# Optimization experiments

Hardware: AMD Instinct MI355X
Metric: run time of the kernel (lower is better)

Reference implementation:

```python
import jax, jax.numpy as jnp
import numpy as np

B, T, ENC, TAG, HG, HE, M = 64, 383, 768, 128, 400, 256, 20
D = ENC + TAG          # graph RNN input size (encoder_output_dim + tag_representation_dim)
S = T + 1              # +1 for head sentinel


def setup_inputs() -> dict:
    ks = jax.random.split(jax.random.key(0), 16)
    g = lambda i, shape, s=0.05: jax.random.normal(ks[i], shape, dtype=jnp.float32) * s
    z = lambda n: jnp.zeros((n,), jnp.float32)
    return dict(
        input=g(0, (B, T, ENC), 1.0),
        tag_embeddings=g(1, (B, T, TAG), 1.0),
        mask=jnp.ones((B, T), jnp.int32),
        head_sentinel=g(2, (D,), 1.0),
        # bidirectional graph RNN (tanh, 1 layer)
        Wih_f=g(3, (HG, D)), Whh_f=g(4, (HG, HG)), bih_f=z(HG), bhh_f=z(HG),
        Wih_b=g(5, (HG, D)), Whh_b=g(6, (HG, HG)), bih_b=z(HG), bhh_b=z(HG),
        # graph_to_edge projection (edge RNN initial hidden)
        Wg2e=g(7, (HE, 2 * HG)), bg2e=z(HE),
        # edge RNN (past direction, input size 1) + edge classifier head
        Wih_e=g(8, (HE, 1)), Whh_e=g(9, (HE, HE)), bih_e=z(HE), bhh_e=z(HE),
        Wcls=g(10, (1, HE)), bcls=z(1),
        bos=z(1),
        # head/dep tag feedforwards
        Wht=g(11, (TAG, 2 * HG)), bht=z(TAG),
        Wdt=g(12, (TAG, 2 * HG)), bdt=z(TAG),
    )


def _masked_rnn(x, m, Wih, Whh, bih, bhh, reverse):
    # x: [B,S,D], m: [B,S,1]. Emulates packed nn.RNN(tanh) for one direction:
    # hidden only advances on valid steps (so the backward direction starts its
    # recurrence at each sequence's true length), outputs are zero on padding
    # (matching pad_packed_sequence zero padding).
    def step(h, inp):
        xt, mt = inp
        hn = jnp.tanh(xt @ Wih.T + bih + h @ Whh.T + bhh)
        h = mt * hn + (1.0 - mt) * h
        return h, h * mt

    h0 = jnp.zeros((x.shape[0], Wih.shape[0]), x.dtype)
    _, ys = jax.lax.scan(step, h0, (x.swapaxes(0, 1), m.swapaxes(0, 1)), reverse=reverse)
    return ys.swapaxes(0, 1)


def reference(input, tag_embeddings, mask, head_sentinel,
              Wih_f, Whh_f, bih_f, bhh_f, Wih_b, Whh_b, bih_b, bhh_b,
              Wg2e, bg2e, Wih_e, Whh_e, bih_e, bhh_e, Wcls, bcls, bos,
              Wht, bht, Wdt, bdt):
    x = jnp.concatenate([input, tag_embeddings], axis=-1)            # [B,T,D]
    sent = jnp.broadcast_to(head_sentinel, (B, 1, D))
    x = jnp.concatenate([sent, x], axis=1)                           # [B,S,D]
    m = jnp.concatenate([jnp.ones((B, 1), mask.dtype), mask], axis=1)  # sentinel is valid
    mf = m.astype(x.dtype)[..., None]                                # [B,S,1]

    fwd = _masked_rnn(x, mf, Wih_f, Whh_f, bih_f, bhh_f, reverse=False)
    bwd = _masked_rnn(x, mf, Wih_b, Whh_b, bih_b, bhh_b, reverse=True)
    graph_state = jnp.concatenate([fwd, bwd], axis=-1)               # [B,S,2*HG]

    # initial hidden = graph_to_edge(graph_state), input starts at bos, then
    # feeds back the previous logit.
    proj = graph_state.reshape(B * S, 2 * HG) @ Wg2e.T + bg2e        # [B*S,HE]
    steps = min(M, S)
    x0 = jnp.broadcast_to(bos.reshape(1, 1), (B * S, 1))

    def estep(carry, _):
        xe, h = carry
        hn = jnp.tanh(xe @ Wih_e.T + bih_e + h @ Whh_e.T + bhh_e)
        logit = hn @ Wcls.T + bcls                                   # [B*S,1]
        return (logit, hn), logit

    _, logits = jax.lax.scan(estep, (x0, proj), None, length=steps)  # [steps,B*S,1]
    Ap = logits.squeeze(-1).T.reshape(B, S, steps)                   # [B,S,steps]

    # banded scatter: arc_logits[:, i, start:i] = Ap[:, i, :i-start], start=max(0,i-M)
    rows = jnp.arange(S)[:, None]
    cols = jnp.arange(S)[None, :]
    start = jnp.maximum(0, rows - M)
    k = cols - start
    valid = (cols >= start) & (cols < rows)
    idx = jnp.clip(k, 0, steps - 1)
    band = Ap[:, jnp.broadcast_to(rows, (S, S)), jnp.broadcast_to(idx, (S, S))]  # [B,S,S]
    arc_logits = jnp.where(valid[None], band, jnp.zeros((), Ap.dtype))

    # tag feedforwards (Dropout is identity in eval)
    head_tag = jax.nn.elu(graph_state @ Wht.T + bht)
    dep_tag = jax.nn.elu(graph_state @ Wdt.T + bdt)
    return head_tag, dep_tag, arc_logits
```

## Files before the change

kernel.cpp:

```cpp
#include <hip/hip_runtime.h>

#define B_ 64
#define T_ 383
#define S_ 384
#define ENC_ 768
#define TAGD_ 128
#define D_ 896
#define HG_ 400
#define HE_ 256
#define MSTEP_ 20
#define RTOT_ (B_*S_)
#define HEAD_SZ_ ((size_t)RTOT_*TAGD_)

typedef short short8 __attribute__((ext_vector_type(8)));
typedef float f32x4 __attribute__((ext_vector_type(4)));

__device__ __forceinline__ float bf2f(unsigned short u){
  union { unsigned int i; float f; } v; v.i = ((unsigned int)u) << 16; return v.f;
}
__device__ __forceinline__ unsigned short f2bf(float f){
  union { float f; unsigned int i; } v; v.f = f;
  unsigned int r = (v.i + 0x7fffu + ((v.i >> 16) & 1u)) >> 16;
  return (unsigned short)r;
}
__device__ __forceinline__ float tanh_fast(float x){
  float xc = fminf(fmaxf(x, -15.f), 15.f);
  float e = __expf(2.f*xc);
  return (e - 1.f) * __builtin_amdgcn_rcpf(e + 1.f);
}

__device__ __forceinline__ void probe_maps(int lane, int* mlab, int* nlab){
  unsigned short lb = f2bf((float)(lane & 15));
  short8 av, bv;
  #pragma unroll
  for (int j = 0; j < 8; j++){ av[j] = (short)lb; bv[j] = (short)0x3F80; }
  f32x4 z = {0.f,0.f,0.f,0.f};
  f32x4 d1 = __builtin_amdgcn_mfma_f32_16x16x32_bf16(av, bv, z, 0, 0, 0);
  f32x4 d2 = __builtin_amdgcn_mfma_f32_16x16x32_bf16(bv, av, z, 0, 0, 0);
  #pragma unroll
  for (int i = 0; i < 4; i++){
    mlab[i] = (int)(d1[i]*0.03125f + 0.5f);
    nlab[i] = (int)(d2[i]*0.03125f + 0.5f);
  }
}

__global__ __launch_bounds__(256) void cvt4(const float* __restrict__ src,
                                            unsigned short* __restrict__ dst, int n4)
{
  int i = blockIdx.x*256 + threadIdx.x;
  if (i >= n4) return;
  float4 v = ((const float4*)src)[i];
  ((ushort4*)dst)[i] = make_ushort4(f2bf(v.x), f2bf(v.y), f2bf(v.z), f2bf(v.w));
}

__global__ __launch_bounds__(256) void pack_wrnn3(const float* __restrict__ Wf,
                                                  const float* __restrict__ Wb,
                                                  unsigned short* __restrict__ Wr)
{
  int idx = blockIdx.x*256 + threadIdx.x;
  if (idx >= 2*26*13*16*32) return;
  int dir = idx / (26*13*16*32);
  int rem = idx % (26*13*16*32);
  int tile = rem / (13*16*32); rem %= (13*16*32);
  int kt = rem / (16*32);      rem %= (16*32);
  int r  = rem / 32;
  int kk = rem % 32;
  int n = tile*16 + r, k = kt*32 + kk;
  unsigned short v = 0;
  if (n < HG_ && k < HG_) v = f2bf((dir ? Wb : Wf)[(size_t)n*HG_ + k]);
  Wr[idx] = v;
}

__global__ __launch_bounds__(64) void maskpack(const int* __restrict__ mask,
                                               unsigned long long* __restrict__ mb)
{
  int t = blockIdx.x; int b = threadIdx.x;
  int m = (t > 0) ? mask[b*T_ + (t-1)] : 1;
  unsigned long long v = __ballot(m != 0);
  if (b == 0) mb[t] = v;
}

__global__ __launch_bounds__(256) void gemm_pre(
    const float* __restrict__ inp, const float* __restrict__ tag,
    const float* __restrict__ sent, const unsigned short* __restrict__ W,
    const float* __restrict__ bihf, const float* __restrict__ bhhf,
    const float* __restrict__ bihb, const float* __restrict__ bhhb,
    unsigned short* __restrict__ preT2)
{
  int wid = blockIdx.x*4 + (threadIdx.x >> 6);
  int lane = threadIdx.x & 63;
  int q = lane >> 4, l16 = lane & 15;
  int mt = wid / 25, ct = wid % 25;
  int r = mt*16 + l16;
  int s = r % S_, b = r / S_;
  int mlab[4], nlab[4];
  probe_maps(lane, mlab, nlab);
  int n0 = ct*32 + l16, n1 = n0 + 16;
  const unsigned short* w0 = W + (size_t)n0*D_;
  const unsigned short* w1 = W + (size_t)n1*D_;
  f32x4 acc0 = {0.f,0.f,0.f,0.f}, acc1 = {0.f,0.f,0.f,0.f};
  for (int k0 = 0; k0 < D_; k0 += 32){
    int k = k0 + q*8;
    const float* asrc = (s == 0) ? (sent + k)
        : ((k < ENC_) ? inp + (size_t)(b*T_ + (s-1))*ENC_ + k
                      : tag + (size_t)(b*T_ + (s-1))*TAGD_ + (k - ENC_));
    float4 v0 = *(const float4*)asrc;
    float4 v1 = *(const float4*)(asrc + 4);
    short8 a;
    a[0]=(short)f2bf(v0.x); a[1]=(short)f2bf(v0.y); a[2]=(short)f2bf(v0.z); a[3]=(short)f2bf(v0.w);
    a[4]=(short)f2bf(v1.x); a[5]=(short)f2bf(v1.y); a[6]=(short)f2bf(v1.z); a[7]=(short)f2bf(v1.w);
    acc0 = __builtin_amdgcn_mfma_f32_16x16x32_bf16(a, *(const short8*)(w0 + k), acc0, 0,0,0);
    acc1 = __builtin_amdgcn_mfma_f32_16x16x32_bf16(a, *(const short8*)(w1 + k), acc1, 0,0,0);
  }
  #pragma unroll
  for (int i = 0; i < 4; i++){
    int row = mt*16 + mlab[i];
    int c0 = ct*32 + nlab[i], c1 = c0 + 16;
    int bb = row / S_, ss = row % S_;
    int mtb = bb >> 4, qb = (bb >> 2) & 3, rib = bb & 3;
    float v0 = acc0[i] + ((c0 < HG_) ? (bihf[c0] + bhhf[c0]) : (bihb[c0-HG_] + bhhb[c0-HG_]));
    float v1 = acc1[i] + ((c1 < HG_) ? (bihf[c1] + bhhf[c1]) : (bihb[c1-HG_] + bhhb[c1-HG_]));
    {
      int d = (c0 >= HG_) ? 1 : 0; int nn = c0 - d*HG_;
      int nt = nn >> 4, lc = nn & 15;
      preT2[((((size_t)(d*S_ + ss)*25 + nt)*4 + mtb)*64 + (qb*16 + lc))*4 + rib] = f2bf(v0);
    }
    {
      int d = (c1 >= HG_) ? 1 : 0; int nn = c1 - d*HG_;
      int nt = nn >> 4, lc = nn & 15;
      preT2[((((size_t)(d*S_ + ss)*25 + nt)*4 + mtb)*64 + (qb*16 + lc))*4 + rib] = f2bf(v1);
    }
  }
}

#define HSTR5_ 424
template<int NTC>
__device__ void rnn_body5(int nt0, int dir, int bg, int lane, int tid,
    const unsigned short* __restrict__ pD,
    const unsigned short* __restrict__ Wd,
    const unsigned long long* __restrict__ mbits,
    unsigned short* __restrict__ gs,
    unsigned short (*Hh)[HSTR5_], unsigned short (*Hl)[HSTR5_])
{
  int q = lane >> 4, l16 = lane & 15;
  const unsigned short* wrow[NTC];
  #pragma unroll
  for (int j = 0; j < NTC; j++)
    wrow[j] = Wd + (size_t)(nt0 + j)*13*512 + l16*32 + q*8;

  short8 bh[NTC][6];
  #pragma unroll
  for (int j = 0; j < NTC; j++)
    #pragma unroll
    for (int kt = 0; kt < 6; kt++)
      bh[j][kt] = *(const short8*)(wrow[j] + kt*512);

  for (int stp = 0; stp < S_; stp++){
    int t = dir ? (S_ - 1 - stp) : stp;
    unsigned long long mb = mbits[t];
    bool allm = (mb == 0xFFFFFFFFFFFFFFFFull);
    const unsigned short* pT = pD + (size_t)t*25600;

    ushort4 pu[NTC];
    #pragma unroll
    for (int j = 0; j < NTC; j++)
      pu[j] = *(const ushort4*)(pT + (((size_t)(nt0 + j)*4 + bg)*64 + lane)*4);

    f32x4 acc[NTC];
    #pragma unroll
    for (int j = 0; j < NTC; j++) acc[j] = (f32x4){0.f,0.f,0.f,0.f};

    #pragma unroll
    for (int kt = 6; kt < 13; kt++){
      short8 bv[NTC];
      #pragma unroll
      for (int j = 0; j < NTC; j++) bv[j] = *(const short8*)(wrow[j] + kt*512);
      short8 ah = *(const short8*)&Hh[l16][kt*32 + q*8];
      short8 al = *(const short8*)&Hl[l16][kt*32 + q*8];
      #pragma unroll
      for (int j = 0; j < NTC; j++){
        acc[j] = __builtin_amdgcn_mfma_f32_16x16x32_bf16(ah, bv[j], acc[j], 0,0,0);
        acc[j] = __builtin_amdgcn_mfma_f32_16x16x32_bf16(al, bv[j], acc[j], 0,0,0);
      }
    }
    #pragma unroll
    for (int kt = 0; kt < 6; kt++){
      short8 ah = *(const short8*)&Hh[l16][kt*32 + q*8];
      short8 al = *(const short8*)&Hl[l16][kt*32 + q*8];
      #pragma unroll
      for (int j = 0; j < NTC; j++){
        acc[j] = __builtin_amdgcn_mfma_f32_16x16x32_bf16(ah, bh[j][kt], acc[j], 0,0,0);
        acc[j] = __builtin_amdgcn_mfma_f32_16x16x32_bf16(al, bh[j][kt], acc[j], 0,0,0);
      }
    }

    __syncthreads();

    #pragma unroll
    for (int j = 0; j < NTC; j++){
      int n = (nt0 + j)*16 + l16;
      unsigned short pv[4] = {pu[j].x, pu[j].y, pu[j].z, pu[j].w};
      #pragma unroll
      for (int ri = 0; ri < 4; ri++){
        int b = q*4 + ri;
        float hn = tanh_fast(acc[j][ri] + bf2f(pv[ri]));
        float hnew;
        if (allm) hnew = hn;
        else {
          bool mv = (mb >> (bg*16 + b)) & 1ull;
          float hold = bf2f(Hh[b][n]) + bf2f(Hl[b][n]);
          hnew = mv ? hn : hold;
        }
        unsigned short hi = f2bf(hnew);
        Hh[b][n] = hi;
        Hl[b][n] = f2bf(hnew - bf2f(hi));
      }
    }
    __syncthreads();

    for (int c = tid; c < 800; c += 512){
      int b = c / 50, off = c - b*50;
      uint4 dv = *(const uint4*)&Hh[b][off*8];
      bool mv = (mb >> (bg*16 + b)) & 1ull;
      uint4 z = make_uint4(0,0,0,0);
      *(uint4*)(gs + (size_t)((bg*16 + b)*S_ + t)*800 + dir*HG_ + off*8) = mv ? dv : z;
    }
  }
}

__global__ __launch_bounds__(512, 1) void rnn_mfma5(
    const unsigned short* __restrict__ preT2, const unsigned short* __restrict__ Wr,
    const unsigned long long* __restrict__ mbits, unsigned short* __restrict__ gs)
{
  __shared__ __align__(16) unsigned short Hh[16][HSTR5_];
  __shared__ __align__(16) unsigned short Hl[16][HSTR5_];
  int tid = threadIdx.x;
  int wave = tid >> 6, lane = tid & 63;
  int dir = blockIdx.x >> 2, bg = blockIdx.x & 3;
  for (int i = tid; i < 16*HSTR5_/2; i += 512){
    ((unsigned int*)Hh)[i] = 0u;
    ((unsigned int*)Hl)[i] = 0u;
  }
  __syncthreads();
  const unsigned short* Wd = Wr + (size_t)dir*26*13*512;
  const unsigned short* pD = preT2 + (size_t)dir*S_*25600;
  if (wave == 0) rnn_body5<4>(0,                dir, bg, lane, tid, pD, Wd, mbits, gs, Hh, Hl);
  else           rnn_body5<3>(4 + (wave-1)*3,   dir, bg, lane, tid, pD, Wd, mbits, gs, Hh, Hl);
}

__global__ __launch_bounds__(256) void gemm_proj(
    const unsigned short* __restrict__ gs, const unsigned short* __restrict__ Wg2e,
    const float* __restrict__ bg2e, float* __restrict__ proj)
{
  int wid = blockIdx.x*4 + (threadIdx.x >> 6);
  int lane = threadIdx.x & 63;
  int q = lane >> 4, l16 = lane & 15;
  int mt = wid >> 3, ct = wid & 7;
  int mlab[4], nlab[4];
  probe_maps(lane, mlab, nlab);
  const unsigned short* arow = gs + (size_t)(mt*16 + l16)*800;
  int n0 = ct*32 + l16, n1 = n0 + 16;
  const unsigned short* w0 = Wg2e + (size_t)n0*800;
  const unsigned short* w1 = Wg2e + (size_t)n1*800;
  f32x4 acc0 = {0.f,0.f,0.f,0.f}, acc1 = {0.f,0.f,0.f,0.f};
  for (int k0 = 0; k0 < 800; k0 += 32){
    int k = k0 + q*8;
    short8 a = *(const short8*)(arow + k);
    acc0 = __builtin_amdgcn_mfma_f32_16x16x32_bf16(a, *(const short8*)(w0 + k), acc0, 0,0,0);
    acc1 = __builtin_amdgcn_mfma_f32_16x16x32_bf16(a, *(const short8*)(w1 + k), acc1, 0,0,0);
  }
  #pragma unroll
  for (int i = 0; i < 4; i++){
    int row = mt*16 + mlab[i];
    int c0 = ct*32 + nlab[i], c1 = c0 + 16;
    proj[(size_t)row*HE_ + c0] = acc0[i] + bg2e[c0];
    proj[(size_t)row*HE_ + c1] = acc1[i] + bg2e[c1];
  }
}

__global__ __launch_bounds__(256) void gemm_tag(
    const unsigned short* __restrict__ gs, const unsigned short* __restrict__ Wtag,
    const float* __restrict__ bht, const float* __restrict__ bdt,
    float* __restrict__ outH)
{
  int wid = blockIdx.x*4 + (threadIdx.x >> 6);
  int lane = threadIdx.x & 63;
  int q = lane >> 4, l16 = lane & 15;
  int mt = wid >> 3, ct = wid & 7;
  int mlab[4], nlab[4];
  probe_maps(lane, mlab, nlab);
  const unsigned short* arow = gs + (size_t)(mt*16 + l16)*800;
  int n0 = ct*32 + l16, n1 = n0 + 16;
  const unsigned short* w0 = Wtag + (size_t)n0*800;
  const unsigned short* w1 = Wtag + (size_t)n1*800;
  f32x4 acc0 = {0.f,0.f,0.f,0.f}, acc1 = {0.f,0.f,0.f,0.f};
  for (int k0 = 0; k0 < 800; k0 += 32){
    int k = k0 + q*8;
    short8 a = *(const short8*)(arow + k);
    acc0 = __builtin_amdgcn_mfma_f32_16x16x32_bf16(a, *(const short8*)(w0 + k), acc0, 0,0,0);
    acc1 = __builtin_amdgcn_mfma_f32_16x16x32_bf16(a, *(const short8*)(w1 + k), acc1, 0,0,0);
  }
  #pragma unroll
  for (int i = 0; i < 4; i++){
    int row = mt*16 + mlab[i];
    int c0 = ct*32 + nlab[i], c1 = c0 + 16;
    float v0 = acc0[i] + ((c0 < TAGD_) ? bht[c0] : bdt[c0-TAGD_]);
    float v1 = acc1[i] + ((c1 < TAGD_) ? bht[c1] : bdt[c1-TAGD_]);
    v0 = (v0 > 0.f) ? v0 : expm1f(v0);
    v1 = (v1 > 0.f) ? v1 : expm1f(v1);
    if (c0 < TAGD_) outH[(size_t)row*TAGD_ + c0] = v0;
    else            outH[HEAD_SZ_ + (size_t)row*TAGD_ + (c0-TAGD_)] = v0;
    if (c1 < TAGD_) outH[(size_t)row*TAGD_ + c1] = v1;
    else            outH[HEAD_SZ_ + (size_t)row*TAGD_ + (c1-TAGD_)] = v1;
  }
}

#define EROWS_ 96
#define ESTR_ 264
__global__ __launch_bounds__(256, 1) void estep2(
    const float* __restrict__ proj, const unsigned short* __restrict__ WhhE,
    const float* __restrict__ bihE, const float* __restrict__ bhhE,
    const float* __restrict__ WihE, const float* __restrict__ Wcls,
    const float* __restrict__ bclsp, const float* __restrict__ bosp,
    float* __restrict__ Ap)
{
  __shared__ __align__(16) unsigned short H[2][EROWS_][ESTR_];
  __shared__ float lacc[4][EROWS_];
  __shared__ float xls[EROWS_];
  int tid = threadIdx.x;
  int wave = tid >> 6, lane = tid & 63, q = lane >> 4, l16 = lane & 15;
  size_t rowbase = (size_t)blockIdx.x * EROWS_;

  short8 bw[4][8];
  float bias_n[4], wcl_n[4], wih_n[4];
  #pragma unroll
  for (int nt = 0; nt < 4; nt++){
    int n = wave*64 + nt*16 + l16;
    #pragma unroll
    for (int kt = 0; kt < 8; kt++)
      bw[nt][kt] = *(const short8*)(WhhE + (size_t)n*HE_ + kt*32 + q*8);
    bias_n[nt] = bihE[n] + bhhE[n];
    wcl_n[nt]  = Wcls[n];
    wih_n[nt]  = WihE[n];
  }
  for (int i = tid; i < EROWS_*HE_; i += 256){
    int r = i >> 8, n = i & 255;
    H[0][r][n] = f2bf(proj[(rowbase + r)*HE_ + n]);
  }
  if (tid < EROWS_) xls[tid] = bosp[0];
  float bc = bclsp[0];
  __syncthreads();

  for (int stp = 0; stp < MSTEP_; stp++){
    int cur = stp & 1, nxt = cur ^ 1;
    float lp[6][4];
    #pragma unroll
    for (int mt = 0; mt < 6; mt++){
      short8 af[8];
      #pragma unroll
      for (int kt = 0; kt < 8; kt++)
        af[kt] = *(const short8*)&H[cur][mt*16 + l16][kt*32 + q*8];
      float xr[4];
      #pragma unroll
      for (int ri = 0; ri < 4; ri++) xr[ri] = xls[mt*16 + q*4 + ri];
      f32x4 acc[4];
      #pragma unroll
      for (int nt = 0; nt < 4; nt++) acc[nt] = (f32x4){0.f,0.f,0.f,0.f};
      #pragma unroll
      for (int kt = 0; kt < 8; kt++){
        #pragma unroll
        for (int nt = 0; nt < 4; nt++)
          acc[nt] = __builtin_amdgcn_mfma_f32_16x16x32_bf16(af[kt], bw[nt][kt], acc[nt], 0,0,0);
      }
      #pragma unroll
      for (int ri = 0; ri < 4; ri++) lp[mt][ri] = 0.f;
      #pragma unroll
      for (int nt = 0; nt < 4; nt++){
        int n = wave*64 + nt*16 + l16;
        #pragma unroll
        for (int ri = 0; ri < 4; ri++){
          float v = acc[nt][ri] + bias_n[nt] + xr[ri]*wih_n[nt];
          float h = tanh_fast(v);
          lp[mt][ri] += h * wcl_n[nt];
          H[nxt][mt*16 + q*4 + ri][n] = f2bf(h);
        }
      }
    }
    #pragma unroll
    for (int mt = 0; mt < 6; mt++){
      #pragma unroll
      for (int ri = 0; ri < 4; ri++){
        float v = lp[mt][ri];
        v += __shfl_xor(v, 1, 16);
        v += __shfl_xor(v, 2, 16);
        v += __shfl_xor(v, 4, 16);
        v += __shfl_xor(v, 8, 16);
        lp[mt][ri] = v;
      }
    }
    if (l16 == 0){
      #pragma unroll
      for (int mt = 0; mt < 6; mt++)
        #pragma unroll
        for (int ri = 0; ri < 4; ri++)
          lacc[wave][mt*16 + q*4 + ri] = lp[mt][ri];
    }
    __syncthreads();
    if (tid < EROWS_){
      float lg = lacc[0][tid] + lacc[1][tid] + lacc[2][tid] + lacc[3][tid] + bc;
      Ap[(rowbase + tid)*MSTEP_ + stp] = lg;
      xls[tid] = lg;
    }
    __syncthreads();
  }
}

__global__ __launch_bounds__(256) void band_kernel(const float* __restrict__ Ap,
                                                   float* __restrict__ arc)
{
  int idx = blockIdx.x*256 + threadIdx.x;
  int c = idx % S_;
  int rr = (idx / S_) % S_;
  int b = idx / (S_*S_);
  int start = rr - MSTEP_; if (start < 0) start = 0;
  bool valid = (c >= start) && (c < rr);
  float v = 0.f;
  if (valid) v = Ap[(size_t)(b*S_ + rr)*MSTEP_ + (c - start)];
  arc[idx] = v;
}

extern "C" void kernel_launch(void* const* d_in, const int* in_sizes, int n_in,
                              void* d_out, int out_size, void* d_ws, size_t ws_size,
                              hipStream_t stream)
{
  const float* inp  = (const float*)d_in[0];
  const float* tag  = (const float*)d_in[1];
  const int*   mask = (const int*)d_in[2];
  const float* sent = (const float*)d_in[3];
  const float* Wihf = (const float*)d_in[4];
  const float* Whhf = (const float*)d_in[5];
  const float* bihf = (const float*)d_in[6];
  const float* bhhf = (const float*)d_in[7];
  const float* Wihb = (const float*)d_in[8];
  const float* Whhb = (const float*)d_in[9];
  const float* bihb = (const float*)d_in[10];
  const float* bhhb = (const float*)d_in[11];
  const float* Wg2e = (const float*)d_in[12];
  const float* bg2e = (const float*)d_in[13];
  const float* WihE = (const float*)d_in[14];
  const float* WhhE = (const float*)d_in[15];
  const float* bihE = (const float*)d_in[16];
  const float* bhhE = (const float*)d_in[17];
  const float* Wcls = (const float*)d_in[18];
  const float* bcls = (const float*)d_in[19];
  const float* bos  = (const float*)d_in[20];
  const float* Wht  = (const float*)d_in[21];
  const float* bht  = (const float*)d_in[22];
  const float* Wdt  = (const float*)d_in[23];
  const float* bdt  = (const float*)d_in[24];
  (void)in_sizes; (void)n_in; (void)out_size; (void)ws_size;

  char* ws = (char*)d_ws;
  unsigned short* preT2  = (unsigned short*)ws;
  unsigned short* gs     = (unsigned short*)(ws + 39321600);
  unsigned short* Wrnn3  = (unsigned short*)(ws + 78643200);
  unsigned short* Wihcat = (unsigned short*)(ws + 79335424);
  unsigned short* Wg2e_b = (unsigned short*)(ws + 80769024);
  unsigned short* Wtag_b = (unsigned short*)(ws + 81178624);
  unsigned short* WhhE_b = (unsigned short*)(ws + 81588224);
  unsigned long long* maskb = (unsigned long long*)(ws + 81719296);
  float*          proj   = (float*)ws;
  float*          Ap     = (float*)(ws + 25165824);

  float* outH   = (float*)d_out;
  float* outArc = outH + 2*HEAD_SZ_;

  hipLaunchKernelGGL(cvt4, dim3(350), dim3(256), 0, stream, Wihf, Wihcat,           400*896/4);
  hipLaunchKernelGGL(cvt4, dim3(350), dim3(256), 0, stream, Wihb, Wihcat + 400*896, 400*896/4);
  hipLaunchKernelGGL(cvt4, dim3(200), dim3(256), 0, stream, Wg2e, Wg2e_b,           256*800/4);
  hipLaunchKernelGGL(cvt4, dim3(100), dim3(256), 0, stream, Wht,  Wtag_b,           128*800/4);
  hipLaunchKernelGGL(cvt4, dim3(100), dim3(256), 0, stream, Wdt,  Wtag_b + 128*800, 128*800/4);
  hipLaunchKernelGGL(cvt4, dim3(64),  dim3(256), 0, stream, WhhE, WhhE_b,           256*256/4);
  hipLaunchKernelGGL(pack_wrnn3, dim3(1352), dim3(256), 0, stream, Whhf, Whhb, Wrnn3);
  hipLaunchKernelGGL(maskpack, dim3(S_), dim3(64), 0, stream, mask, maskb);
  hipLaunchKernelGGL(gemm_pre, dim3(9600), dim3(256), 0, stream,
                     inp, tag, sent, Wihcat, bihf, bhhf, bihb, bhhb, preT2);
  hipLaunchKernelGGL(rnn_mfma5, dim3(8), dim3(512), 0, stream, preT2, Wrnn3, maskb, gs);
  hipLaunchKernelGGL(gemm_proj, dim3(3072), dim3(256), 0, stream, gs, Wg2e_b, bg2e, proj);
  hipLaunchKernelGGL(gemm_tag,  dim3(3072), dim3(256), 0, stream, gs, Wtag_b, bht, bdt, outH);
  hipLaunchKernelGGL(estep2, dim3(256), dim3(256), 0, stream,
                     proj, WhhE_b, bihE, bhhE, WihE, Wcls, bcls, bos, Ap);
  hipLaunchKernelGGL(band_kernel, dim3(36864), dim3(256), 0, stream, Ap, outArc);
}
```

Before: 2.284 ms.

## Remap pre-GEMM rows, XOR-swizzle RNN LDS, halve estep rows per block

The input-projection GEMM now indexes tiles time-major so each 16-row tile holds 16 batches at one timestep. That lets it write the RNN-friendly preT2 layout with one vectorized ushort4 store per column, and it uses packed hardware bf16 conversion. The recurrent kernel's LDS hidden-state arrays switch to a 512-wide stride with an XOR swizzle to avoid bank conflicts on the MFMA operand reads. The edge-RNN kernel handles 48 rows per block over twice as many blocks to improve occupancy and parallelism.

```diff
diff --git a/kernel.cpp b/kernel.cpp
--- a/kernel.cpp
+++ b/kernel.cpp
@@ -91,8 +91,8 @@
   int lane = threadIdx.x & 63;
   int q = lane >> 4, l16 = lane & 15;
   int mt = wid / 25, ct = wid % 25;
-  int r = mt*16 + l16;
-  int s = r % S_, b = r / S_;
+  int t = mt >> 2, mtb = mt & 3;
+  int b = mtb*16 + l16;
   int mlab[4], nlab[4];
   probe_maps(lane, mlab, nlab);
   int n0 = ct*32 + l16, n1 = n0 + 16;
@@ -101,46 +101,50 @@
   f32x4 acc0 = {0.f,0.f,0.f,0.f}, acc1 = {0.f,0.f,0.f,0.f};
   for (int k0 = 0; k0 < D_; k0 += 32){
     int k = k0 + q*8;
-    const float* asrc = (s == 0) ? (sent + k)
-        : ((k < ENC_) ? inp + (size_t)(b*T_ + (s-1))*ENC_ + k
-                      : tag + (size_t)(b*T_ + (s-1))*TAGD_ + (k - ENC_));
+    const float* asrc = (t == 0) ? (sent + k)
+        : ((k < ENC_) ? inp + (size_t)(b*T_ + (t-1))*ENC_ + k
+                      : tag + (size_t)(b*T_ + (t-1))*TAGD_ + (k - ENC_));
     float4 v0 = *(const float4*)asrc;
     float4 v1 = *(const float4*)(asrc + 4);
-    short8 a;
-    a[0]=(short)f2bf(v0.x); a[1]=(short)f2bf(v0.y); a[2]=(short)f2bf(v0.z); a[3]=(short)f2bf(v0.w);
-    a[4]=(short)f2bf(v1.x); a[5]=(short)f2bf(v1.y); a[6]=(short)f2bf(v1.z); a[7]=(short)f2bf(v1.w);
+    union { unsigned int u[4]; short8 s8; } au;
+    asm("v_cvt_pk_bf16_f32 %0, %1, %2" : "=v"(au.u[0]) : "v"(v0.x), "v"(v0.y));
+    asm("v_cvt_pk_bf16_f32 %0, %1, %2" : "=v"(au.u[1]) : "v"(v0.z), "v"(v0.w));
+    asm("v_cvt_pk_bf16_f32 %0, %1, %2" : "=v"(au.u[2]) : "v"(v1.x), "v"(v1.y));
+    asm("v_cvt_pk_bf16_f32 %0, %1, %2" : "=v"(au.u[3]) : "v"(v1.z), "v"(v1.w));
+    short8 a = au.s8;
     acc0 = __builtin_amdgcn_mfma_f32_16x16x32_bf16(a, *(const short8*)(w0 + k), acc0, 0,0,0);
     acc1 = __builtin_amdgcn_mfma_f32_16x16x32_bf16(a, *(const short8*)(w1 + k), acc1, 0,0,0);
   }
+  int q0 = mlab[0] >> 2;
+  float bb0 = (n0 < HG_) ? (bihf[n0] + bhhf[n0]) : (bihb[n0-HG_] + bhhb[n0-HG_]);
+  float bb1 = (n1 < HG_) ? (bihf[n1] + bhhf[n1]) : (bihb[n1-HG_] + bhhb[n1-HG_]);
+  unsigned short v0[4], v1[4];
   #pragma unroll
   for (int i = 0; i < 4; i++){
-    int row = mt*16 + mlab[i];
-    int c0 = ct*32 + nlab[i], c1 = c0 + 16;
-    int bb = row / S_, ss = row % S_;
-    int mtb = bb >> 4, qb = (bb >> 2) & 3, rib = bb & 3;
-    float v0 = acc0[i] + ((c0 < HG_) ? (bihf[c0] + bhhf[c0]) : (bihb[c0-HG_] + bhhb[c0-HG_]));
-    float v1 = acc1[i] + ((c1 < HG_) ? (bihf[c1] + bhhf[c1]) : (bihb[c1-HG_] + bhhb[c1-HG_]));
-    {
-      int d = (c0 >= HG_) ? 1 : 0; int nn = c0 - d*HG_;
-      int nt = nn >> 4, lc = nn & 15;
-      preT2[((((size_t)(d*S_ + ss)*25 + nt)*4 + mtb)*64 + (qb*16 + lc))*4 + rib] = f2bf(v0);
-    }
-    {
-      int d = (c1 >= HG_) ? 1 : 0; int nn = c1 - d*HG_;
-      int nt = nn >> 4, lc = nn & 15;
-      preT2[((((size_t)(d*S_ + ss)*25 + nt)*4 + mtb)*64 + (qb*16 + lc))*4 + rib] = f2bf(v1);
-    }
-  }
-}
-
-#define HSTR5_ 424
+    v0[mlab[i] & 3] = f2bf(acc0[i] + bb0);
+    v1[mlab[i] & 3] = f2bf(acc1[i] + bb1);
+  }
+  {
+    int d = (n0 >= HG_) ? 1 : 0; int nn = n0 - d*HG_; int nt = nn >> 4;
+    size_t slab = (((size_t)(d*S_ + t)*25 + nt)*4 + mtb)*256;
+    *(ushort4*)(preT2 + slab + (q0*16 + l16)*4) = make_ushort4(v0[0], v0[1], v0[2], v0[3]);
+  }
+  {
+    int d = (n1 >= HG_) ? 1 : 0; int nn = n1 - d*HG_; int nt = nn >> 4;
+    size_t slab = (((size_t)(d*S_ + t)*25 + nt)*4 + mtb)*256;
+    *(ushort4*)(preT2 + slab + (q0*16 + l16)*4) = make_ushort4(v1[0], v1[1], v1[2], v1[3]);
+  }
+}
+
+#define HSTR9_ 512
+#define HX(row, col) ((col) ^ (((row) & 15) << 3))
 template<int NTC>
-__device__ void rnn_body5(int nt0, int dir, int bg, int lane, int tid,
+__device__ void rnn_body9(int nt0, int dir, int bg, int lane, int tid,
     const unsigned short* __restrict__ pD,
     const unsigned short* __restrict__ Wd,
     const unsigned long long* __restrict__ mbits,
     unsigned short* __restrict__ gs,
-    unsigned short (*Hh)[HSTR5_], unsigned short (*Hl)[HSTR5_])
+    unsigned short (*Hh)[HSTR9_], unsigned short (*Hl)[HSTR9_])
 {
   int q = lane >> 4, l16 = lane & 15;
   const unsigned short* wrow[NTC];
@@ -175,8 +179,8 @@
       short8 bv[NTC];
       #pragma unroll
       for (int j = 0; j < NTC; j++) bv[j] = *(const short8*)(wrow[j] + kt*512);
-      short8 ah = *(const short8*)&Hh[l16][kt*32 + q*8];
-      short8 al = *(const short8*)&Hl[l16][kt*32 + q*8];
+      short8 ah = *(const short8*)&Hh[l16][HX(l16, kt*32 + q*8)];
+      short8 al = *(const short8*)&Hl[l16][HX(l16, kt*32 + q*8)];
       #pragma unroll
       for (int j = 0; j < NTC; j++){
         acc[j] = __builtin_amdgcn_mfma_f32_16x16x32_bf16(ah, bv[j], acc[j], 0,0,0);
@@ -185,8 +189,8 @@
     }
     #pragma unroll
     for (int kt = 0; kt < 6; kt++){
-      short8 ah = *(const short8*)&Hh[l16][kt*32 + q*8];
-      short8 al = *(const short8*)&Hl[l16][kt*32 + q*8];
+      short8 ah = *(const short8*)&Hh[l16][HX(l16, kt*32 + q*8)];
+      short8 al = *(const short8*)&Hl[l16][HX(l16, kt*32 + q*8)];
       #pragma unroll
       for (int j = 0; j < NTC; j++){
         acc[j] = __builtin_amdgcn_mfma_f32_16x16x32_bf16(ah, bh[j][kt], acc[j], 0,0,0);
@@ -208,19 +212,19 @@
         if (allm) hnew = hn;
         else {
           bool mv = (mb >> (bg*16 + b)) & 1ull;
-          float hold = bf2f(Hh[b][n]) + bf2f(Hl[b][n]);
+          float hold = bf2f(Hh[b][HX(b, n)]) + bf2f(Hl[b][HX(b, n)]);
           hnew = mv ? hn : hold;
         }
         unsigned short hi = f2bf(hnew);
-        Hh[b][n] = hi;
-        Hl[b][n] = f2bf(hnew - bf2f(hi));
+        Hh[b][HX(b, n)] = hi;
+        Hl[b][HX(b, n)] = f2bf(hnew - bf2f(hi));
       }
     }
     __syncthreads();
 
     for (int c = tid; c < 800; c += 512){
       int b = c / 50, off = c - b*50;
-      uint4 dv = *(const uint4*)&Hh[b][off*8];
+      uint4 dv = *(const uint4*)&Hh[b][HX(b, off*8)];
       bool mv = (mb >> (bg*16 + b)) & 1ull;
       uint4 z = make_uint4(0,0,0,0);
       *(uint4*)(gs + (size_t)((bg*16 + b)*S_ + t)*800 + dir*HG_ + off*8) = mv ? dv : z;
@@ -228,24 +232,24 @@
   }
 }
 
-__global__ __launch_bounds__(512, 1) void rnn_mfma5(
+__global__ __launch_bounds__(512, 1) void rnn_mfma9(
     const unsigned short* __restrict__ preT2, const unsigned short* __restrict__ Wr,
     const unsigned long long* __restrict__ mbits, unsigned short* __restrict__ gs)
 {
-  __shared__ __align__(16) unsigned short Hh[16][HSTR5_];
-  __shared__ __align__(16) unsigned short Hl[16][HSTR5_];
+  __shared__ __align__(16) unsigned short Hh[16][HSTR9_];
+  __shared__ __align__(16) unsigned short Hl[16][HSTR9_];
   int tid = threadIdx.x;
   int wave = tid >> 6, lane = tid & 63;
   int dir = blockIdx.x >> 2, bg = blockIdx.x & 3;
-  for (int i = tid; i < 16*HSTR5_/2; i += 512){
+  for (int i = tid; i < 16*HSTR9_/2; i += 512){
     ((unsigned int*)Hh)[i] = 0u;
     ((unsigned int*)Hl)[i] = 0u;
   }
   __syncthreads();
   const unsigned short* Wd = Wr + (size_t)dir*26*13*512;
   const unsigned short* pD = preT2 + (size_t)dir*S_*25600;
-  if (wave == 0) rnn_body5<4>(0,                dir, bg, lane, tid, pD, Wd, mbits, gs, Hh, Hl);
-  else           rnn_body5<3>(4 + (wave-1)*3,   dir, bg, lane, tid, pD, Wd, mbits, gs, Hh, Hl);
+  if (wave == 0) rnn_body9<4>(0,                dir, bg, lane, tid, pD, Wd, mbits, gs, Hh, Hl);
+  else           rnn_body9<3>(4 + (wave-1)*3,   dir, bg, lane, tid, pD, Wd, mbits, gs, Hh, Hl);
 }
 
 __global__ __launch_bounds__(256) void gemm_proj(
@@ -315,7 +319,7 @@
   }
 }
 
-#define EROWS_ 96
+#define EROWS_ 48
 #define ESTR_ 264
 __global__ __launch_bounds__(256, 1) void estep2(
     const float* __restrict__ proj, const unsigned short* __restrict__ WhhE,
@@ -353,9 +357,9 @@
 
   for (int stp = 0; stp < MSTEP_; stp++){
     int cur = stp & 1, nxt = cur ^ 1;
-    float lp[6][4];
-    #pragma unroll
-    for (int mt = 0; mt < 6; mt++){
+    float lp[3][4];
+    #pragma unroll
+    for (int mt = 0; mt < 3; mt++){
       short8 af[8];
       #pragma unroll
       for (int kt = 0; kt < 8; kt++)
@@ -387,7 +391,7 @@
       }
     }
     #pragma unroll
-    for (int mt = 0; mt < 6; mt++){
+    for (int mt = 0; mt < 3; mt++){
       #pragma unroll
       for (int ri = 0; ri < 4; ri++){
         float v = lp[mt][ri];
@@ -400,7 +404,7 @@
     }
     if (l16 == 0){
       #pragma unroll
-      for (int mt = 0; mt < 6; mt++)
+      for (int mt = 0; mt < 3; mt++)
         #pragma unroll
         for (int ri = 0; ri < 4; ri++)
           lacc[wave][mt*16 + q*4 + ri] = lp[mt][ri];
@@ -485,10 +489,10 @@
   hipLaunchKernelGGL(maskpack, dim3(S_), dim3(64), 0, stream, mask, maskb);
   hipLaunchKernelGGL(gemm_pre, dim3(9600), dim3(256), 0, stream,
                      inp, tag, sent, Wihcat, bihf, bhhf, bihb, bhhb, preT2);
-  hipLaunchKernelGGL(rnn_mfma5, dim3(8), dim3(512), 0, stream, preT2, Wrnn3, maskb, gs);
+  hipLaunchKernelGGL(rnn_mfma9, dim3(8), dim3(512), 0, stream, preT2, Wrnn3, maskb, gs);
   hipLaunchKernelGGL(gemm_proj, dim3(3072), dim3(256), 0, stream, gs, Wg2e_b, bg2e, proj);
   hipLaunchKernelGGL(gemm_tag,  dim3(3072), dim3(256), 0, stream, gs, Wtag_b, bht, bdt, outH);
-  hipLaunchKernelGGL(estep2, dim3(256), dim3(256), 0, stream,
+  hipLaunchKernelGGL(estep2, dim3(512), dim3(256), 0, stream,
                      proj, WhhE_b, bihE, bhhE, WihE, Wcls, bcls, bos, Ap);
   hipLaunchKernelGGL(band_kernel, dim3(36864), dim3(256), 0, stream, Ap, outArc);
 }
```

Measured after the change: 3.324 ms. 45.5% more time.
